# Performance work log

Measured on AMD Instinct MI355X. Metric: run time of the kernel, lower is better.

The kernel has to match this reference:

```python
import jax, jax.numpy as jnp
import numpy as np


def setup_inputs() -> dict:
    key = jax.random.key(0)
    k1, k2, k3, k4 = jax.random.split(key, 4)
    B, K, UNITS, P, Q = 1024, 256, 32, 4, 4
    xavier = float(np.sqrt(6.0 / (K + K)))  # xavier_uniform bound for (k,k) fan
    inputs = jax.random.normal(k1, (B, K, P), dtype=jnp.float32)
    state = jax.random.normal(k2, (B, K * UNITS, Q), dtype=jnp.float32)
    kernel = jax.random.uniform(k3, (P, UNITS, K, K), dtype=jnp.float32, minval=-xavier, maxval=xavier)
    recurrent_kernel = jax.random.uniform(k4, (Q, UNITS, K, K), dtype=jnp.float32, minval=-xavier, maxval=xavier)
    return {"inputs": inputs, "state": state, "kernel": kernel, "recurrent_kernel": recurrent_kernel}


def reference(inputs, state, kernel, recurrent_kernel):
    # inputs: (B, k, p); state: (B, k*units, q)
    # kernel: (p, units, k, k); recurrent_kernel: (q, units, k, k)
    p, units, k, _ = kernel.shape
    q = recurrent_kernel.shape[0]
    B = inputs.shape[0]
    # AR part: sum_p (B,k) @ (units,k,k) -> (B, k_out, units), laid out k-major
    ar = jnp.einsum('bip,puij->bju', inputs, kernel).reshape(B, k * units)
    # MA part: state reshaped (B, k, units, q); per-lag per-unit (B,k)@(k,k)
    st = state.reshape(B, k, units, q)
    ma = jnp.einsum('biuq,quij->bju', st, recurrent_kernel).reshape(B, k * units)
    out = (ar + ma)[:, :, None]  # linear activation, (B, k*units, 1)
    out_state = jnp.concatenate([out, state[:, :, :-1]], axis=-1)  # (B, k*units, q)
    return out, out_state
```

## Files before the change

### kernel.cpp

```cpp
#include <hip/hip_runtime.h>
#include <hip/hip_bf16.h>


typedef __attribute__((ext_vector_type(8))) short bf16x8;
typedef __attribute__((ext_vector_type(4))) float f32x4;

__device__ inline unsigned short f2bf(float x) {
    unsigned int u = __float_as_uint(x);
    return (unsigned short)((u + 0x7fffu + ((u >> 16) & 1u)) >> 16);
}

__device__ inline void cvt_store4(unsigned short* dst, float4 v) {
    float2 ab; ab.x = v.x; ab.y = v.y;
    float2 cd; cd.x = v.z; cd.y = v.w;
    __hip_bfloat162 lo = __float22bfloat162_rn(ab);
    __hip_bfloat162 hi = __float22bfloat162_rn(cd);
    union { __hip_bfloat162 h2[2]; uint2 u2; } pk;
    pk.h2[0] = lo; pk.h2[1] = hi;
    *(uint2*)dst = pk.u2;
}

__device__ inline void cvt_store2(unsigned short* dst, float4 v) {
    float2 ab; ab.x = v.x; ab.y = v.y;
    float2 cd; cd.x = v.z; cd.y = v.w;
    __hip_bfloat162 lo = __float22bfloat162_rn(ab);
    __hip_bfloat162 hi = __float22bfloat162_rn(cd);
    union { __hip_bfloat162 h2[2]; uint2 u2; } pk;
    pk.h2[0] = lo; pk.h2[1] = hi;
    *(uint2*)dst = pk.u2;
}


__global__ __launch_bounds__(256) void prep_w2(
    const float* __restrict__ kern,
    const float* __restrict__ rkern,
    unsigned short* __restrict__ Wtt)
{
    const int u  = blockIdx.x;
    const int j0 = blockIdx.y * 64;
    const int zz = blockIdx.z;
    const int mm = zz >> 4;
    const int it = zz & 15;
    const float* src = mm ? rkern : kern;
    const int kout = mm * 1024 + it * 64;

    __shared__ unsigned short T[64 * 72];

    const int t  = threadIdx.x;
    const int jq = t & 3;
    const int ii = (t >> 2) & 15;
    const int pp = t >> 6;
    const int i  = it * 16 + ii;
    const int kk = ii * 4 + pp;
    const float* row = src + ((size_t)((pp * 32 + u) * 256 + i)) * 256 + j0 + jq * 16;
    #pragma unroll
    for (int s = 0; s < 4; ++s) {
        float4 v = *(const float4*)(row + s * 4);
        const int jb_ = jq * 16 + s * 4;
        T[(jb_ + 0) * 72 + kk] = f2bf(v.x);
        T[(jb_ + 1) * 72 + kk] = f2bf(v.y);
        T[(jb_ + 2) * 72 + kk] = f2bf(v.z);
        T[(jb_ + 3) * 72 + kk] = f2bf(v.w);
    }
    __syncthreads();
    const int j = t >> 2, q = t & 3;
    const int kglob = kout + q * 16;
    const int kt  = kglob >> 5;
    const int kk0 = kglob & 31;
    const int jb  = blockIdx.y >> 1;
    const int jloc = (blockIdx.y & 1) * 64 + j;
    unsigned short* dst = Wtt +
        ((((size_t)(u * 2 + jb) * 64 + kt) * 128 + jloc) * 32 + kk0);
    uint4 a = *(uint4*)&T[j * 72 + q * 16];
    uint4 b = *(uint4*)&T[j * 72 + q * 16 + 8];
    *(uint4*)dst = a;
    *(uint4*)(dst + 8) = b;
}

__global__ __launch_bounds__(256) void prep_a(
    const float* __restrict__ inputs,
    const float* __restrict__ state,
    unsigned short* __restrict__ At_ar,
    unsigned short* __restrict__ At_ma)
{
    const int bid = blockIdx.x;
    if (bid < 512) {
        const size_t e = ((size_t)bid * 256 + threadIdx.x) * 8;
        const int b = (int)(e >> 10), k = (int)(e & 1023);
        float4 v0 = *(const float4*)(inputs + e);
        float4 v1 = *(const float4*)(inputs + e + 4);
        const int mb = b >> 6, row = b & 63, kt = k >> 5, kk = k & 31;
        unsigned short* d = At_ar + (((size_t)(mb * 32 + kt) * 64 + row) * 32 + kk);
        cvt_store4(d, v0);
        cvt_store4(d + 4, v1);
    } else {
        const size_t e4 = (size_t)(bid - 512) * 256 + threadIdx.x;
        const int b = (int)(e4 >> 13), col4 = (int)(e4 & 8191);
        const int i = col4 >> 5, u = col4 & 31;
        float4 v = *(const float4*)(state + e4 * 4);
        const int mb = b >> 6, row = b & 63;
        const int ktp = i >> 3;
        const int kk = (i * 4) & 31;
        unsigned short* d = At_ma +
            ((((size_t)(u * 16 + mb) * 32 + ktp) * 64 + row) * 32 + kk);
        cvt_store2(d, v);
    }
}

#define PITCH 40

__global__ __launch_bounds__(256, 4) void arma_gemm_mfma2(
    const unsigned short* __restrict__ At_ar,
    const unsigned short* __restrict__ At_ma,
    const unsigned short* __restrict__ Wtt,
    float* __restrict__ out)
{
    const int u  = blockIdx.z;
    const int mb = blockIdx.x;
    const int jb = blockIdx.y;
    const int b0 = mb * 64;
    const int j0 = jb * 128;
    const int t  = threadIdx.x;
    const int lane = t & 63;
    const int wn = (t >> 6) * 32;
    const int fm = lane & 15;
    const int kq = lane >> 4;

    __shared__ unsigned short Asr[2][64 * PITCH];
    __shared__ unsigned short Wsr[2][128 * PITCH];

    const int ar_row = t >> 2, ar_off = (t & 3) * 8;
    const int w_row  = t >> 1, w_off  = (t & 1) * 16;

    f32x4 acc[4][2];
    #pragma unroll
    for (int a = 0; a < 4; ++a)
        #pragma unroll
        for (int b = 0; b < 2; ++b)
            acc[a][b] = (f32x4)0.0f;

    const unsigned short* abase_ar = At_ar + (size_t)mb * 32 * 2048 + t * 8;
    const unsigned short* abase_ma = At_ma + (size_t)(u * 16 + mb) * 32 * 2048 + t * 8;
    const unsigned short* wbase    = Wtt + (size_t)(u * 2 + jb) * 64 * 4096 + t * 16;

    uint4 av, w0, w1;

    auto LOAD = [&](int kt) {
        const unsigned short* ta = (kt < 32) ? (abase_ar + (size_t)kt * 2048)
                                             : (abase_ma + (size_t)(kt - 32) * 2048);
        av = *(const uint4*)ta;
        const unsigned short* tw = wbase + (size_t)kt * 4096;
        w0 = *(const uint4*)tw;
        w1 = *(const uint4*)(tw + 2048);
    };
    auto LOADW_FIX = [&](int kt) {
        const unsigned short* tw = wbase + (size_t)kt * 4096;
        w0 = *(const uint4*)tw;
        w1 = *(const uint4*)(tw + 8);
    };
    auto STORE = [&](int buf) {
        *(uint4*)&Asr[buf][ar_row * PITCH + ar_off] = av;
        unsigned short* wd = &Wsr[buf][w_row * PITCH + w_off];
        *(uint4*)wd = w0;
        *(uint4*)(wd + 8) = w1;
    };
    auto COMPUTE = [&](int buf) {
        bf16x8 af[4], bfr[2];
        #pragma unroll
        for (int mt = 0; mt < 4; ++mt)
            af[mt] = *(const bf16x8*)&Asr[buf][(mt * 16 + fm) * PITCH + kq * 8];
        #pragma unroll
        for (int nt = 0; nt < 2; ++nt)
            bfr[nt] = *(const bf16x8*)&Wsr[buf][(wn + nt * 16 + fm) * PITCH + kq * 8];
        #pragma unroll
        for (int mt = 0; mt < 4; ++mt)
            #pragma unroll
            for (int nt = 0; nt < 2; ++nt)
                acc[mt][nt] = __builtin_amdgcn_mfma_f32_16x16x32_bf16(
                    af[mt], bfr[nt], acc[mt][nt], 0, 0, 0);
    };

    {
        const unsigned short* ta = abase_ar;
        av = *(const uint4*)ta;
        LOADW_FIX(0);
    }
    STORE(0);
    __syncthreads();

    int cur = 0;
    for (int kt = 0; kt < 63; ++kt) {
        const int kn = kt + 1;
        const unsigned short* ta = (kn < 32) ? (abase_ar + (size_t)kn * 2048)
                                             : (abase_ma + (size_t)(kn - 32) * 2048);
        av = *(const uint4*)ta;
        LOADW_FIX(kn);
        COMPUTE(cur);
        STORE(cur ^ 1);
        __syncthreads();
        cur ^= 1;
    }
    COMPUTE(cur);

    #pragma unroll
    for (int mt = 0; mt < 4; ++mt) {
        const int rbase = b0 + mt * 16 + kq * 4;
        #pragma unroll
        for (int nt = 0; nt < 2; ++nt) {
            const int col = j0 + wn + nt * 16 + fm;
            float* op = out + (size_t)rbase * 8192 + (size_t)col * 32 + u;
            op[0]        = acc[mt][nt][0];
            op[8192]     = acc[mt][nt][1];
            op[2 * 8192] = acc[mt][nt][2];
            op[3 * 8192] = acc[mt][nt][3];
        }
    }
}

__global__ __launch_bounds__(256) void prep_w(
    const float* __restrict__ kern,
    const float* __restrict__ rkern,
    unsigned short* __restrict__ Wt)
{
    const int u  = blockIdx.x;
    const int j0 = blockIdx.y * 64;
    const int zz = blockIdx.z;
    const int mm = zz >> 4;
    const int it = zz & 15;
    const float* src = mm ? rkern : kern;
    const int kout = mm * 1024 + it * 64;

    __shared__ unsigned short T[64 * 72];

    const int t  = threadIdx.x;
    const int jq = t & 3;
    const int ii = (t >> 2) & 15;
    const int pp = t >> 6;
    const int i  = it * 16 + ii;
    const int kk = ii * 4 + pp;
    const float* row = src + ((size_t)((pp * 32 + u) * 256 + i)) * 256 + j0 + jq * 16;
    #pragma unroll
    for (int s = 0; s < 4; ++s) {
        float4 v = *(const float4*)(row + s * 4);
        const int jb = jq * 16 + s * 4;
        T[(jb + 0) * 72 + kk] = f2bf(v.x);
        T[(jb + 1) * 72 + kk] = f2bf(v.y);
        T[(jb + 2) * 72 + kk] = f2bf(v.z);
        T[(jb + 3) * 72 + kk] = f2bf(v.w);
    }
    __syncthreads();
    const int j = t >> 2, q = t & 3;
    unsigned short* dst = Wt + ((size_t)(u * 256 + j0 + j)) * 2048 + kout + q * 16;
    uint4 a = *(uint4*)&T[j * 72 + q * 16];
    uint4 b = *(uint4*)&T[j * 72 + q * 16 + 8];
    *(uint4*)dst = a;
    *(uint4*)(dst + 8) = b;
}

__global__ __launch_bounds__(256, 4) void arma_gemm_mfma(
    const float* __restrict__ inputs,
    const float* __restrict__ state,
    const unsigned short* __restrict__ Wt,
    float* __restrict__ out)
{
    const int u  = blockIdx.z;
    const int b0 = blockIdx.x * 64;
    const int j0 = blockIdx.y * 128;
    const int t  = threadIdx.x;
    const int lane = t & 63;
    const int wn = (t >> 6) * 32;
    const int fm = lane & 15;
    const int kq = lane >> 4;

    __shared__ unsigned short Asr[2][64 * PITCH];
    __shared__ unsigned short Wsr[2][128 * PITCH];

    const int arow = t & 63;
    const int aseg = t >> 6;
    const int wrow = t >> 1;
    const int wseg = t & 1;

    f32x4 acc[4][2];
    #pragma unroll
    for (int a = 0; a < 4; ++a)
        #pragma unroll
        for (int b = 0; b < 2; ++b)
            acc[a][b] = (f32x4)0.0f;

    const unsigned short* wsrc = Wt + ((size_t)(u * 256 + j0 + wrow)) * 2048 + wseg * 16;
    const float* in_row = inputs + (size_t)(b0 + arow) * 1024 + aseg * 8;
    const float* st_row = state + (size_t)(b0 + arow) * 32768 + (size_t)u * 4;

    float4 a0, a1;
    uint4 w0, w1;

    auto LOAD = [&](int kt) {
        if (kt < 1024) {
            const float* s = in_row + kt;
            a0 = *(const float4*)(s);
            a1 = *(const float4*)(s + 4);
        } else {
            const int kk = kt - 1024 + aseg * 8;
            const float* s = st_row + (size_t)(kk >> 2) * 128;
            a0 = *(const float4*)(s);
            a1 = *(const float4*)(s + 128);
        }
        w0 = *(const uint4*)(wsrc + kt);
        w1 = *(const uint4*)(wsrc + kt + 8);
    };
    auto STORE = [&](int buf) {
        unsigned short* ad = &Asr[buf][arow * PITCH + aseg * 8];
        cvt_store4(ad + 0, a0);
        cvt_store4(ad + 4, a1);
        unsigned short* wd = &Wsr[buf][wrow * PITCH + wseg * 16];
        *(uint4*)wd = w0;
        *(uint4*)(wd + 8) = w1;
    };
    auto COMPUTE = [&](int buf) {
        bf16x8 af[4], bfr[2];
        #pragma unroll
        for (int mt = 0; mt < 4; ++mt)
            af[mt] = *(const bf16x8*)&Asr[buf][(mt * 16 + fm) * PITCH + kq * 8];
        #pragma unroll
        for (int nt = 0; nt < 2; ++nt)
            bfr[nt] = *(const bf16x8*)&Wsr[buf][(wn + nt * 16 + fm) * PITCH + kq * 8];
        #pragma unroll
        for (int mt = 0; mt < 4; ++mt)
            #pragma unroll
            for (int nt = 0; nt < 2; ++nt)
                acc[mt][nt] = __builtin_amdgcn_mfma_f32_16x16x32_bf16(
                    af[mt], bfr[nt], acc[mt][nt], 0, 0, 0);
    };

    LOAD(0);
    STORE(0);
    __syncthreads();

    int cur = 0;
    for (int kt = 0; kt < 2048 - 32; kt += 32) {
        LOAD(kt + 32);
        COMPUTE(cur);
        STORE(cur ^ 1);
        __syncthreads();
        cur ^= 1;
    }
    COMPUTE(cur);

    #pragma unroll
    for (int mt = 0; mt < 4; ++mt) {
        const int rbase = b0 + mt * 16 + kq * 4;
        #pragma unroll
        for (int nt = 0; nt < 2; ++nt) {
            const int col = j0 + wn + nt * 16 + fm;
            float* op = out + (size_t)rbase * 8192 + (size_t)col * 32 + u;
            op[0]        = acc[mt][nt][0];
            op[8192]     = acc[mt][nt][1];
            op[2 * 8192] = acc[mt][nt][2];
            op[3 * 8192] = acc[mt][nt][3];
        }
    }
}

#define BM 64
#define BN 64
#define BKF 16
#define LDP 68

__global__ __launch_bounds__(256) void arma_gemm_f32(
    const float* __restrict__ inputs, const float* __restrict__ state,
    const float* __restrict__ kern, const float* __restrict__ rkern,
    float* __restrict__ out)
{
    const int u = blockIdx.z, b0 = blockIdx.x * BM, j0 = blockIdx.y * BN;
    const int tid = threadIdx.x;
    __shared__ float As[BKF][LDP];
    __shared__ float Ws[BKF][LDP];
    const int tx = tid & 15, ty = tid >> 4;
    const int arow = tid >> 2, ak4 = (tid & 3) * 4;
    const int wrow = tid >> 4, wj = (tid & 15) * 4;
    float acc[4][4] = {{0.f}};
    for (int kt = 0; kt < 1024; kt += BKF) {
        const float4 av = *(const float4*)(inputs + (size_t)(b0 + arow) * 1024 + kt + ak4);
        As[ak4 + 0][arow] = av.x; As[ak4 + 1][arow] = av.y;
        As[ak4 + 2][arow] = av.z; As[ak4 + 3][arow] = av.w;
        const int ip = kt + wrow;
        const float4 wv = *(const float4*)(kern + ((size_t)(((ip & 3) * 32 + u) * 256 + (ip >> 2))) * 256 + j0 + wj);
        *(float4*)&Ws[wrow][wj] = wv;
        __syncthreads();
        #pragma unroll
        for (int kk = 0; kk < BKF; ++kk) {
            const float4 a4 = *(const float4*)&As[kk][ty * 4];
            const float4 w4 = *(const float4*)&Ws[kk][tx * 4];
            acc[0][0] += a4.x * w4.x; acc[0][1] += a4.x * w4.y; acc[0][2] += a4.x * w4.z; acc[0][3] += a4.x * w4.w;
            acc[1][0] += a4.y * w4.x; acc[1][1] += a4.y * w4.y; acc[1][2] += a4.y * w4.z; acc[1][3] += a4.y * w4.w;
            acc[2][0] += a4.z * w4.x; acc[2][1] += a4.z * w4.y; acc[2][2] += a4.z * w4.z; acc[2][3] += a4.z * w4.w;
            acc[3][0] += a4.w * w4.x; acc[3][1] += a4.w * w4.y; acc[3][2] += a4.w * w4.z; acc[3][3] += a4.w * w4.w;
        }
        __syncthreads();
    }
    for (int kt = 0; kt < 1024; kt += BKF) {
        const int i = (kt >> 2) + (tid & 3);
        const float4 av = *(const float4*)(state + (size_t)(b0 + arow) * 32768 + (size_t)(i * 32 + u) * 4);
        As[ak4 + 0][arow] = av.x; As[ak4 + 1][arow] = av.y;
        As[ak4 + 2][arow] = av.z; As[ak4 + 3][arow] = av.w;
        const int iq = kt + wrow;
        const float4 wv = *(const float4*)(rkern + ((size_t)(((iq & 3) * 32 + u) * 256 + (iq >> 2))) * 256 + j0 + wj);
        *(float4*)&Ws[wrow][wj] = wv;
        __syncthreads();
        #pragma unroll
        for (int kk = 0; kk < BKF; ++kk) {
            const float4 a4 = *(const float4*)&As[kk][ty * 4];
            const float4 w4 = *(const float4*)&Ws[kk][tx * 4];
            acc[0][0] += a4.x * w4.x; acc[0][1] += a4.x * w4.y; acc[0][2] += a4.x * w4.z; acc[0][3] += a4.x * w4.w;
            acc[1][0] += a4.y * w4.x; acc[1][1] += a4.y * w4.y; acc[1][2] += a4.y * w4.z; acc[1][3] += a4.y * w4.w;
            acc[2][0] += a4.z * w4.x; acc[2][1] += a4.z * w4.y; acc[2][2] += a4.z * w4.z; acc[2][3] += a4.z * w4.w;
            acc[3][0] += a4.w * w4.x; acc[3][1] += a4.w * w4.y; acc[3][2] += a4.w * w4.z; acc[3][3] += a4.w * w4.w;
        }
        __syncthreads();
    }
    const int bb = b0 + ty * 4, jj = j0 + tx * 4;
    #pragma unroll
    for (int r = 0; r < 4; ++r)
        #pragma unroll
        for (int c = 0; c < 4; ++c)
            out[(size_t)(bb + r) * 8192 + (size_t)(jj + c) * 32 + u] = acc[r][c];
}

__global__ __launch_bounds__(256) void arma_assemble2(
    const float* __restrict__ state,
    const float* __restrict__ out,
    float* __restrict__ out_state)
{
    const size_t i = (size_t)blockIdx.x * 256 + threadIdx.x;
    const f32x4 o = *(const f32x4*)(out + i * 4);
    const float* sp = state + i * 16;
    const f32x4 s0 = *(const f32x4*)(sp + 0);
    const f32x4 s1 = *(const f32x4*)(sp + 4);
    const f32x4 s2 = *(const f32x4*)(sp + 8);
    const f32x4 s3 = *(const f32x4*)(sp + 12);
    f32x4 r0 = { o[0], s0[0], s0[1], s0[2] };
    f32x4 r1 = { o[1], s1[0], s1[1], s1[2] };
    f32x4 r2 = { o[2], s2[0], s2[1], s2[2] };
    f32x4 r3 = { o[3], s3[0], s3[1], s3[2] };
    f32x4* dp = (f32x4*)(out_state + i * 16);
    __builtin_nontemporal_store(r0, dp + 0);
    __builtin_nontemporal_store(r1, dp + 1);
    __builtin_nontemporal_store(r2, dp + 2);
    __builtin_nontemporal_store(r3, dp + 3);
}

extern "C" void kernel_launch(void* const* d_in, const int* in_sizes, int n_in,
                              void* d_out, int out_size, void* d_ws, size_t ws_size,
                              hipStream_t stream) {
    const float* inputs = (const float*)d_in[0];
    const float* state  = (const float*)d_in[1];
    const float* kern   = (const float*)d_in[2];
    const float* rkern  = (const float*)d_in[3];

    float* out       = (float*)d_out;
    float* out_state = (float*)d_out + 8388608;

    const size_t WTT_BYTES  = (size_t)32 * 2 * 64 * 128 * 32 * 2;
    const size_t ATAR_BYTES = (size_t)16 * 32 * 64 * 32 * 2;
    const size_t ATMA_BYTES = (size_t)32 * 16 * 32 * 64 * 32 * 2;
    const size_t NEW_BYTES  = WTT_BYTES + ATAR_BYTES + ATMA_BYTES;
    const size_t WT_BYTES   = (size_t)32 * 256 * 2048 * 2;

    if (ws_size >= NEW_BYTES) {
        unsigned short* Wtt   = (unsigned short*)d_ws;
        unsigned short* At_ar = (unsigned short*)((char*)d_ws + WTT_BYTES);
        unsigned short* At_ma = (unsigned short*)((char*)d_ws + WTT_BYTES + ATAR_BYTES);
        prep_w2<<<dim3(32, 4, 32), 256, 0, stream>>>(kern, rkern, Wtt);
        prep_a<<<dim3(512 + 32768, 1, 1), 256, 0, stream>>>(inputs, state, At_ar, At_ma);
        arma_gemm_mfma2<<<dim3(16, 2, 32), 256, 0, stream>>>(At_ar, At_ma, Wtt, out);
    } else if (ws_size >= WT_BYTES) {
        unsigned short* Wt = (unsigned short*)d_ws;
        prep_w<<<dim3(32, 4, 32), 256, 0, stream>>>(kern, rkern, Wt);
        arma_gemm_mfma<<<dim3(16, 2, 32), 256, 0, stream>>>(inputs, state, Wt, out);
    } else {
        arma_gemm_f32<<<dim3(16, 4, 32), 256, 0, stream>>>(inputs, state, kern, rkern, out);
    }
    arma_assemble2<<<8388608 / 4 / 256, 256, 0, stream>>>(state, out, out_state);
}
```

Measured before the change: 532.1 us.

## Split A prep, tile state transpose via LDS, write GEMM output contiguously then assemble

Splits the A-prep kernel into separate AR and MA kernels. The MA version reads state rows coalesced and transposes them through swizzled shared memory, so the bf16 stores are full 16-byte writes. The GEMM now writes a per-unit contiguous Ct buffer instead of a strided scatter (stride 32 floats) into out. A new assemble kernel then transposes Ct through shared memory and writes out and out_state together. The aim is to remove uncoalesced global writes, at the cost of an extra 32 MB workspace round trip and needing a larger workspace.

```diff
diff --git a/kernel.cpp b/kernel.cpp
--- a/kernel.cpp
+++ b/kernel.cpp
@@ -75,6 +75,185 @@
     uint4 b = *(uint4*)&T[j * 72 + q * 16 + 8];
     *(uint4*)dst = a;
     *(uint4*)(dst + 8) = b;
+}
+
+__global__ __launch_bounds__(256) void prep_a_ar(
+    const float* __restrict__ inputs,
+    unsigned short* __restrict__ At_ar)
+{
+    const size_t e = ((size_t)blockIdx.x * 256 + threadIdx.x) * 8;
+    const int b = (int)(e >> 10), k = (int)(e & 1023);
+    float4 v0 = *(const float4*)(inputs + e);
+    float4 v1 = *(const float4*)(inputs + e + 4);
+    const int mb = b >> 6, row = b & 63, kt = k >> 5, kk = k & 31;
+    unsigned short* d = At_ar + (((size_t)(mb * 32 + kt) * 64 + row) * 32 + kk);
+    cvt_store4(d, v0);
+    cvt_store4(d + 4, v1);
+}
+
+__global__ __launch_bounds__(256) void prep_a_ma(
+    const float* __restrict__ state,
+    unsigned short* __restrict__ At_ma)
+{
+    const int bt  = blockIdx.x;
+    const int ktp = blockIdx.y;
+    const int t = threadIdx.x;
+    __shared__ unsigned short L[32 * 16 * 40];
+
+    const int r = t >> 4;
+    const int l = t & 15;
+    const float* src = state + (size_t)(bt * 16 + r) * 32768 + ktp * 1024 + l * 4;
+    #pragma unroll
+    for (int s = 0; s < 16; ++s) {
+        float4 v = *(const float4*)(src + s * 64);
+        const int c4   = l + s * 16;
+        const int u    = c4 & 31;
+        const int iloc = c4 >> 5;
+        const int slot = iloc ^ (u & 7);
+        cvt_store2(&L[(u * 16 + r) * 40 + slot * 4], v);
+    }
+    __syncthreads();
+    const int mb   = bt >> 2;
+    const int row0 = (bt & 3) * 16;
+    const int part = t & 3;
+    #pragma unroll
+    for (int w = 0; w < 8; ++w) {
+        const int pI = w * 64 + (t >> 2);
+        const int u  = pI >> 4;
+        const int rr = pI & 15;
+        const int s0 = (2 * part) ^ (u & 7);
+        const int s1 = (2 * part + 1) ^ (u & 7);
+        uint2 d0 = *(const uint2*)&L[(u * 16 + rr) * 40 + s0 * 4];
+        uint2 d1 = *(const uint2*)&L[(u * 16 + rr) * 40 + s1 * 4];
+        uint4 o; o.x = d0.x; o.y = d0.y; o.z = d1.x; o.w = d1.y;
+        unsigned short* dst = At_ma +
+            ((((size_t)(u * 16 + mb) * 32 + ktp) * 64 + (row0 + rr)) * 32 + part * 8);
+        *(uint4*)dst = o;
+    }
+}
+
+#define PITCH 40
+
+__global__ __launch_bounds__(256, 4) void arma_gemm_mfma2ct(
+    const unsigned short* __restrict__ At_ar,
+    const unsigned short* __restrict__ At_ma,
+    const unsigned short* __restrict__ Wtt,
+    float* __restrict__ Ct)
+{
+    const int u  = blockIdx.z;
+    const int mb = blockIdx.x;
+    const int jb = blockIdx.y;
+    const int b0 = mb * 64;
+    const int j0 = jb * 128;
+    const int t  = threadIdx.x;
+    const int lane = t & 63;
+    const int wn = (t >> 6) * 32;
+    const int fm = lane & 15;
+    const int kq = lane >> 4;
+
+    __shared__ unsigned short Asr[2][64 * PITCH];
+    __shared__ unsigned short Wsr[2][128 * PITCH];
+
+    const int ar_row = t >> 2, ar_off = (t & 3) * 8;
+    const int w_row  = t >> 1, w_off  = (t & 1) * 16;
+
+    f32x4 acc[4][2];
+    #pragma unroll
+    for (int a = 0; a < 4; ++a)
+        #pragma unroll
+        for (int b = 0; b < 2; ++b)
+            acc[a][b] = (f32x4)0.0f;
+
+    const unsigned short* abase_ar = At_ar + (size_t)mb * 32 * 2048 + t * 8;
+    const unsigned short* abase_ma = At_ma + (size_t)(u * 16 + mb) * 32 * 2048 + t * 8;
+    const unsigned short* wbase    = Wtt + (size_t)(u * 2 + jb) * 64 * 4096 + t * 16;
+
+    uint4 av, w0, w1;
+
+    auto LOADW = [&](int kt) {
+        const unsigned short* tw = wbase + (size_t)kt * 4096;
+        w0 = *(const uint4*)tw;
+        w1 = *(const uint4*)(tw + 8);
+    };
+    auto STORE = [&](int buf) {
+        *(uint4*)&Asr[buf][ar_row * PITCH + ar_off] = av;
+        unsigned short* wd = &Wsr[buf][w_row * PITCH + w_off];
+        *(uint4*)wd = w0;
+        *(uint4*)(wd + 8) = w1;
+    };
+    auto COMPUTE = [&](int buf) {
+        bf16x8 af[4], bfr[2];
+        #pragma unroll
+        for (int mt = 0; mt < 4; ++mt)
+            af[mt] = *(const bf16x8*)&Asr[buf][(mt * 16 + fm) * PITCH + kq * 8];
+        #pragma unroll
+        for (int nt = 0; nt < 2; ++nt)
+            bfr[nt] = *(const bf16x8*)&Wsr[buf][(wn + nt * 16 + fm) * PITCH + kq * 8];
+        #pragma unroll
+        for (int mt = 0; mt < 4; ++mt)
+            #pragma unroll
+            for (int nt = 0; nt < 2; ++nt)
+                acc[mt][nt] = __builtin_amdgcn_mfma_f32_16x16x32_bf16(
+                    af[mt], bfr[nt], acc[mt][nt], 0, 0, 0);
+    };
+
+    av = *(const uint4*)abase_ar;
+    LOADW(0);
+    STORE(0);
+    __syncthreads();
+
+    int cur = 0;
+    for (int kt = 0; kt < 63; ++kt) {
+        const int kn = kt + 1;
+        const unsigned short* ta = (kn < 32) ? (abase_ar + (size_t)kn * 2048)
+                                             : (abase_ma + (size_t)(kn - 32) * 2048);
+        av = *(const uint4*)ta;
+        LOADW(kn);
+        COMPUTE(cur);
+        STORE(cur ^ 1);
+        __syncthreads();
+        cur ^= 1;
+    }
+    COMPUTE(cur);
+
+    #pragma unroll
+    for (int mt = 0; mt < 4; ++mt) {
+        const int rbase = b0 + mt * 16 + kq * 4;
+        #pragma unroll
+        for (int nt = 0; nt < 2; ++nt) {
+            const int col = j0 + wn + nt * 16 + fm;
+            float* op = Ct + (size_t)u * 262144 + (size_t)rbase * 256 + col;
+            op[0]       = acc[mt][nt][0];
+            op[256]     = acc[mt][nt][1];
+            op[2 * 256] = acc[mt][nt][2];
+            op[3 * 256] = acc[mt][nt][3];
+        }
+    }
+}
+
+__global__ __launch_bounds__(256) void arma_assemble3(
+    const float* __restrict__ state,
+    const float* __restrict__ Ct,
+    float* __restrict__ out,
+    float* __restrict__ out_state)
+{
+    const int b = blockIdx.x;
+    const int t = threadIdx.x;
+    __shared__ float L[256 * 33];
+    for (int u = 0; u < 32; ++u)
+        L[t * 33 + u] = Ct[((size_t)u * 1024 + b) * 256 + t];
+    __syncthreads();
+    const float* srow = state + (size_t)b * 32768;
+    float* orow  = out + (size_t)b * 8192;
+    float* osrow = out_state + (size_t)b * 32768;
+    for (int w = 0; w < 32; ++w) {
+        const int n = w * 256 + t;
+        const float o = L[(n >> 5) * 33 + (n & 31)];
+        const f32x4 s = *(const f32x4*)(srow + (size_t)n * 4);
+        __builtin_nontemporal_store(o, orow + n);
+        f32x4 rv = { o, s[0], s[1], s[2] };
+        __builtin_nontemporal_store(rv, (f32x4*)(osrow + (size_t)n * 4));
+    }
 }
 
 __global__ __launch_bounds__(256) void prep_a(
@@ -107,8 +286,6 @@
     }
 }
 
-#define PITCH 40
-
 __global__ __launch_bounds__(256, 4) void arma_gemm_mfma2(
     const unsigned short* __restrict__ At_ar,
     const unsigned short* __restrict__ At_ma,
@@ -145,15 +322,7 @@
 
     uint4 av, w0, w1;
 
-    auto LOAD = [&](int kt) {
-        const unsigned short* ta = (kt < 32) ? (abase_ar + (size_t)kt * 2048)
-                                             : (abase_ma + (size_t)(kt - 32) * 2048);
-        av = *(const uint4*)ta;
-        const unsigned short* tw = wbase + (size_t)kt * 4096;
-        w0 = *(const uint4*)tw;
-        w1 = *(const uint4*)(tw + 2048);
-    };
-    auto LOADW_FIX = [&](int kt) {
+    auto LOADW = [&](int kt) {
         const unsigned short* tw = wbase + (size_t)kt * 4096;
         w0 = *(const uint4*)tw;
         w1 = *(const uint4*)(tw + 8);
@@ -180,11 +349,8 @@
                     af[mt], bfr[nt], acc[mt][nt], 0, 0, 0);
     };
 
-    {
-        const unsigned short* ta = abase_ar;
-        av = *(const uint4*)ta;
-        LOADW_FIX(0);
-    }
+    av = *(const uint4*)abase_ar;
+    LOADW(0);
     STORE(0);
     __syncthreads();
 
@@ -194,7 +360,7 @@
         const unsigned short* ta = (kn < 32) ? (abase_ar + (size_t)kn * 2048)
                                              : (abase_ma + (size_t)(kn - 32) * 2048);
         av = *(const uint4*)ta;
-        LOADW_FIX(kn);
+        LOADW(kn);
         COMPUTE(cur);
         STORE(cur ^ 1);
         __syncthreads();
@@ -463,22 +629,36 @@
     const size_t WTT_BYTES  = (size_t)32 * 2 * 64 * 128 * 32 * 2;
     const size_t ATAR_BYTES = (size_t)16 * 32 * 64 * 32 * 2;
     const size_t ATMA_BYTES = (size_t)32 * 16 * 32 * 64 * 32 * 2;
-    const size_t NEW_BYTES  = WTT_BYTES + ATAR_BYTES + ATMA_BYTES;
+    const size_t CT_BYTES   = (size_t)32 * 1024 * 256 * 4;
+    const size_t R2_BYTES   = WTT_BYTES + ATAR_BYTES + ATMA_BYTES;
+    const size_t R3_BYTES   = R2_BYTES + CT_BYTES;
     const size_t WT_BYTES   = (size_t)32 * 256 * 2048 * 2;
 
-    if (ws_size >= NEW_BYTES) {
+    if (ws_size >= R3_BYTES) {
+        unsigned short* Wtt   = (unsigned short*)d_ws;
+        unsigned short* At_ar = (unsigned short*)((char*)d_ws + WTT_BYTES);
+        unsigned short* At_ma = (unsigned short*)((char*)d_ws + WTT_BYTES + ATAR_BYTES);
+        float* Ct             = (float*)((char*)d_ws + R2_BYTES);
+        prep_w2<<<dim3(32, 4, 32), 256, 0, stream>>>(kern, rkern, Wtt);
+        prep_a_ar<<<dim3(512), 256, 0, stream>>>(inputs, At_ar);
+        prep_a_ma<<<dim3(64, 32), 256, 0, stream>>>(state, At_ma);
+        arma_gemm_mfma2ct<<<dim3(16, 2, 32), 256, 0, stream>>>(At_ar, At_ma, Wtt, Ct);
+        arma_assemble3<<<dim3(1024), 256, 0, stream>>>(state, Ct, out, out_state);
+    } else if (ws_size >= R2_BYTES) {
         unsigned short* Wtt   = (unsigned short*)d_ws;
         unsigned short* At_ar = (unsigned short*)((char*)d_ws + WTT_BYTES);
         unsigned short* At_ma = (unsigned short*)((char*)d_ws + WTT_BYTES + ATAR_BYTES);
         prep_w2<<<dim3(32, 4, 32), 256, 0, stream>>>(kern, rkern, Wtt);
         prep_a<<<dim3(512 + 32768, 1, 1), 256, 0, stream>>>(inputs, state, At_ar, At_ma);
         arma_gemm_mfma2<<<dim3(16, 2, 32), 256, 0, stream>>>(At_ar, At_ma, Wtt, out);
+        arma_assemble2<<<8388608 / 4 / 256, 256, 0, stream>>>(state, out, out_state);
     } else if (ws_size >= WT_BYTES) {
         unsigned short* Wt = (unsigned short*)d_ws;
         prep_w<<<dim3(32, 4, 32), 256, 0, stream>>>(kern, rkern, Wt);
         arma_gemm_mfma<<<dim3(16, 2, 32), 256, 0, stream>>>(inputs, state, Wt, out);
+        arma_assemble2<<<8388608 / 4 / 256, 256, 0, stream>>>(state, out, out_state);
     } else {
         arma_gemm_f32<<<dim3(16, 4, 32), 256, 0, stream>>>(inputs, state, kern, rkern, out);
-    }
-    arma_assemble2<<<8388608 / 4 / 256, 256, 0, stream>>>(state, out, out_state);
-}
+        arma_assemble2<<<8388608 / 4 / 256, 256, 0, stream>>>(state, out, out_state);
+    }
+}
```

Measured after the change: 440.4 us. -17.2%, faster.
